# Kernel optimization log

Hardware: AMD Instinct MI355X
Metric: run time of the kernel (lower is better)

## Reference

```python
import jax, jax.numpy as jnp
import numpy as np

NUM_GROUPS = 32
EPS = 1e-5


def setup_inputs() -> dict:
    key = jax.random.key(0)
    ks = jax.random.split(key, 3)
    B, C, H, W = 4, 128, 64, 64
    x = jax.random.normal(ks[0], (B, C, H, W), dtype=jnp.float32)
    norm_w = jnp.ones((C,), jnp.float32)
    norm_b = jnp.zeros((C,), jnp.float32)
    qkv_w = jax.random.normal(ks[1], (3 * C, C), dtype=jnp.float32) * (C ** -0.5)
    qkv_b = jnp.zeros((3 * C,), jnp.float32)
    proj_w = jax.random.normal(ks[2], (C, C), dtype=jnp.float32) * (C ** -0.5)
    proj_b = jnp.zeros((C,), jnp.float32)
    return {"x": x, "norm_w": norm_w, "norm_b": norm_b,
            "qkv_w": qkv_w, "qkv_b": qkv_b,
            "proj_w": proj_w, "proj_b": proj_b}


def group_norm(x, w, b):
    B, C, H, W = x.shape
    xg = x.reshape(B, NUM_GROUPS, -1)  # [B, G, (C/G)*H*W]
    mean = jnp.mean(xg, axis=-1, keepdims=True)
    var = jnp.var(xg, axis=-1, keepdims=True)
    h = ((xg - mean) * jax.lax.rsqrt(var + EPS)).reshape(B, C, H, W)
    return h * w[None, :, None, None] + b[None, :, None, None]


def reference(x, norm_w, norm_b, qkv_w, qkv_b, proj_w, proj_b):
    B, C, H, W = x.shape
    N = H * W
    scale = C ** -0.5
    h = group_norm(x, norm_w, norm_b)
    # 1x1 conv == per-pixel matmul over channels
    qkv = jnp.einsum('bchw,dc->bdhw', h, qkv_w) + qkv_b[None, :, None, None]
    q, k, v = jnp.split(qkv.reshape(B, 3 * C, N), 3, axis=1)  # each [B, C, N]
    attn = jax.nn.softmax(jnp.einsum('bcn,bcm->bnm', q, k) * scale, axis=-1)  # [B,N,N]
    out = jnp.einsum('bnm,bcm->bcn', attn, v).reshape(B, C, H, W)
    out = jnp.einsum('bchw,dc->bdhw', out, proj_w) + proj_b[None, :, None, None]
    return x + out
```

## Files before the change

### kernel.cpp

```cpp
#include <hip/hip_runtime.h>
#include <hip/hip_bf16.h>

typedef __attribute__((ext_vector_type(8))) short short8_t;
typedef __attribute__((ext_vector_type(4))) float f32x4_t;
typedef __attribute__((ext_vector_type(16))) float f32x16_t;
typedef __attribute__((ext_vector_type(2))) unsigned int uint2v_t;
typedef __attribute__((ext_vector_type(4))) unsigned int uint4v_t;

#define MFMA16(a, b, c) __builtin_amdgcn_mfma_f32_16x16x32_bf16((a), (b), (c), 0, 0, 0)
#define MFMA32(a, b, c) __builtin_amdgcn_mfma_f32_32x32x16_bf16((a), (b), (c), 0, 0, 0)

__device__ __forceinline__ unsigned short f2bf(float f) {
  unsigned int u = __float_as_uint(f);
  unsigned int r = (u + 0x7fffu + ((u >> 16) & 1u)) >> 16;
  return (unsigned short)r;
}
__device__ __forceinline__ float bf2f(unsigned short u) {
  return __uint_as_float(((unsigned int)u) << 16);
}

__device__ __forceinline__ unsigned int cvt_pk_bf16(float lo, float hi) {
  unsigned int r;
  asm("v_cvt_pk_bf16_f32 %0, %1, %2" : "=v"(r) : "v"(lo), "v"(hi));
  return r;
}

__device__ __forceinline__ float ex2(float x) {
  float r;
  asm("v_exp_f32 %0, %1" : "=v"(r) : "v"(x));
  return r;
}

__device__ __forceinline__ void gload_lds16(const void* g, void* l) {
  __builtin_amdgcn_global_load_lds(
      (const __attribute__((address_space(1))) unsigned int*)g,
      (__attribute__((address_space(3))) unsigned int*)l, 16, 0, 0);
}

__device__ __forceinline__ void stage_gload_256(const char* __restrict__ g,
                                                char* lds, int nchunks,
                                                int wg, int nw, int lane) {
  for (int c = wg; c < nchunks; c += nw) {
    int row = c * 4 + (lane >> 4);
    int srco = row * 256 + ((((lane & 15) << 4)) ^ ((row & 7) << 4));
    gload_lds16(g + srco, lds + c * 1024);
  }
}

#define NB 4
#define NC 128
#define NN 4096
#define NG 32
#define NS 6
#define ATT_SCALE 0.08838834764831843f
#define QSCALE (0.08838834764831843f * 1.4426950408889634f)
#define FIXED_MAX2 14.426950408889634f

__global__ __launch_bounds__(256) void gn_stats_convw(const float* __restrict__ x,
                                                      const float* __restrict__ qkv_w,
                                                      const float* __restrict__ proj_w,
                                                      float* __restrict__ mean,
                                                      float* __restrict__ rstd,
                                                      unsigned short* __restrict__ wq,
                                                      unsigned short* __restrict__ wp) {
  if (blockIdx.x >= 128) {
    int i = (blockIdx.x - 128) * 256 + threadIdx.x;
    if (i < 384 * 128) wq[i] = f2bf(qkv_w[i]);
    if (i < 128 * 128) wp[i] = f2bf(proj_w[i]);
    return;
  }
  int bg = blockIdx.x;
  const float4* p = (const float4*)(x + (size_t)bg * 16384);
  float s = 0.f, ss = 0.f;
  for (int i = threadIdx.x; i < 4096; i += 256) {
    float4 v = p[i];
    s += v.x + v.y + v.z + v.w;
    ss += v.x * v.x + v.y * v.y + v.z * v.z + v.w * v.w;
  }
#pragma unroll
  for (int off = 32; off >= 1; off >>= 1) {
    s += __shfl_down(s, off);
    ss += __shfl_down(ss, off);
  }
  __shared__ float sb[4], ssb[4];
  int w = threadIdx.x >> 6;
  if ((threadIdx.x & 63) == 0) { sb[w] = s; ssb[w] = ss; }
  __syncthreads();
  if (threadIdx.x == 0) {
    float ts = sb[0] + sb[1] + sb[2] + sb[3];
    float tss = ssb[0] + ssb[1] + ssb[2] + ssb[3];
    float m = ts * (1.f / 16384.f);
    float var = tss * (1.f / 16384.f) - m * m;
    mean[bg] = m;
    rstd[bg] = rsqrtf(var + 1e-5f);
  }
}

__global__ __launch_bounds__(256) void qkv_gemm(const float* __restrict__ x,
                                                const float* __restrict__ mean,
                                                const float* __restrict__ rstd,
                                                const float* __restrict__ gw,
                                                const float* __restrict__ gb,
                                                const unsigned short* __restrict__ wq,
                                                const float* __restrict__ bias,
                                                unsigned short* __restrict__ q_t,
                                                unsigned short* __restrict__ k_t,
                                                unsigned short* __restrict__ v) {
  __shared__ __align__(16) char As[384 * 256];
  __shared__ __align__(16) char Bs[64 * 256];
  __shared__ __align__(16) unsigned short T[128 * 72];
  int nt = blockIdx.x, b = blockIdx.y;
  int tid = threadIdx.x, l = tid & 63, wgv = tid >> 6;
  int n0 = nt * 64;

  stage_gload_256((const char*)wq, As, 96, wgv, 4, l);

  {
    int c = tid >> 1, half = tid & 1;
    int g = c >> 2;
    float m = mean[b * NG + g], rs = rstd[b * NG + g];
    float sc = gw[c] * rs, off = gb[c] - m * sc;
    const float4* xr = (const float4*)(x + (size_t)b * NC * NN + (size_t)c * NN + n0 + half * 32);
    unsigned short* tr = T + c * 72 + half * 32;
#pragma unroll
    for (int j = 0; j < 8; ++j) {
      float4 vv = xr[j];
      unsigned int p0 = (unsigned int)f2bf(vv.x * sc + off) |
                        ((unsigned int)f2bf(vv.y * sc + off) << 16);
      unsigned int p1 = (unsigned int)f2bf(vv.z * sc + off) |
                        ((unsigned int)f2bf(vv.w * sc + off) << 16);
      *(unsigned int*)(tr + j * 4) = p0;
      *(unsigned int*)(tr + j * 4 + 2) = p1;
    }
  }
  __syncthreads();

  for (int u = tid; u < 1024; u += 256) {
    int n = u >> 4, slot = u & 15;
    int c0 = slot * 8;
    uint4 packed;
    packed.x = (unsigned int)T[(c0 + 0) * 72 + n] | ((unsigned int)T[(c0 + 1) * 72 + n] << 16);
    packed.y = (unsigned int)T[(c0 + 2) * 72 + n] | ((unsigned int)T[(c0 + 3) * 72 + n] << 16);
    packed.z = (unsigned int)T[(c0 + 4) * 72 + n] | ((unsigned int)T[(c0 + 5) * 72 + n] << 16);
    packed.w = (unsigned int)T[(c0 + 6) * 72 + n] | ((unsigned int)T[(c0 + 7) * 72 + n] << 16);
    *(uint4*)(Bs + n * 256 + ((slot << 4) ^ ((n & 7) << 4))) = packed;
  }
  __syncthreads();

  int w = tid >> 6;
  int arow0 = w * 32 + (l & 15);
  int brow0 = (l & 15);
  int kbyte0 = (l >> 4) * 16;
  int rbase = (l >> 4) * 4;
  int cl = l & 15;

#pragma unroll
  for (int dt = 0; dt < 3; ++dt) {
    const char* Ad = As + dt * 32768;
    f32x4_t acc[2][4] = {};
#pragma unroll
    for (int kk = 0; kk < 4; ++kk) {
      int kb = kk * 64 + kbyte0;
      short8_t aF[2], bF[4];
#pragma unroll
      for (int mi = 0; mi < 2; ++mi) {
        int r = arow0 + mi * 16;
        aF[mi] = *(const short8_t*)(Ad + r * 256 + (kb ^ ((r & 7) << 4)));
      }
#pragma unroll
      for (int ni = 0; ni < 4; ++ni) {
        int r = brow0 + ni * 16;
        bF[ni] = *(const short8_t*)(Bs + r * 256 + (kb ^ ((r & 7) << 4)));
      }
#pragma unroll
      for (int mi = 0; mi < 2; ++mi)
#pragma unroll
        for (int ni = 0; ni < 4; ++ni)
          acc[mi][ni] = MFMA16(aF[mi], bF[ni], acc[mi][ni]);
    }

#pragma unroll
    for (int mi = 0; mi < 2; ++mi) {
#pragma unroll
      for (int ni = 0; ni < 4; ++ni) {
        int n = n0 + ni * 16 + cl;
#pragma unroll
        for (int r = 0; r < 4; ++r) {
          int d = dt * 128 + w * 32 + mi * 16 + rbase + r;
          float val = acc[mi][ni][r] + bias[d];
          if (dt == 0)
            q_t[((size_t)b * NN + n) * NC + d] = f2bf(val * QSCALE);
          else if (dt == 1)
            k_t[((size_t)b * NN + n) * NC + (d - 128)] = f2bf(val);
          else
            v[((size_t)b * NC + (d - 256)) * NN + n] = f2bf(val);
        }
      }
    }
  }
}

__global__ __launch_bounds__(256) void proj_gemm(const unsigned short* __restrict__ wp,
                                                 const unsigned short* __restrict__ O_p,
                                                 const float* __restrict__ lp,
                                                 const float* __restrict__ bias,
                                                 const float* __restrict__ xres,
                                                 float* __restrict__ out) {
  __shared__ __align__(16) char As[128 * 256];
  __shared__ __align__(16) char Bs[32 * 256];
  __shared__ float invl[32];
  int nt = blockIdx.x, b = blockIdx.z;
  int tid = threadIdx.x, l = tid & 63, wgv = tid >> 6;
  int n0 = nt * 32;

  stage_gload_256((const char*)wp, As, 32, wgv, 4, l);

  if (tid < 32) {
    float ls = 0.f;
#pragma unroll
    for (int s2 = 0; s2 < NS; ++s2)
      ls += lp[(size_t)(b * NS + s2) * NN + n0 + tid];
    invl[tid] = 1.f / ls;
  }
  for (int i = tid; i < 32 * 16; i += 256) {
    int row = i >> 4, sl = i & 15;
    float f[8] = {};
#pragma unroll
    for (int s2 = 0; s2 < NS; ++s2) {
      const unsigned short* p =
          O_p + ((size_t)(b * NS + s2) * NN + n0 + row) * 128 + sl * 8;
      ushort4 u0 = *(const ushort4*)p;
      ushort4 u1 = *(const ushort4*)(p + 4);
      f[0] += bf2f(u0.x); f[1] += bf2f(u0.y); f[2] += bf2f(u0.z); f[3] += bf2f(u0.w);
      f[4] += bf2f(u1.x); f[5] += bf2f(u1.y); f[6] += bf2f(u1.z); f[7] += bf2f(u1.w);
    }
    uint4 packed;
    packed.x = (unsigned int)f2bf(f[0]) | ((unsigned int)f2bf(f[1]) << 16);
    packed.y = (unsigned int)f2bf(f[2]) | ((unsigned int)f2bf(f[3]) << 16);
    packed.z = (unsigned int)f2bf(f[4]) | ((unsigned int)f2bf(f[5]) << 16);
    packed.w = (unsigned int)f2bf(f[6]) | ((unsigned int)f2bf(f[7]) << 16);
    *(uint4*)(Bs + row * 256 + ((sl << 4) ^ ((row & 7) << 4))) = packed;
  }
  __syncthreads();

  int w = tid >> 6;
  f32x4_t acc[2][2] = {};
  int arow0 = w * 32 + (l & 15);
  int brow0 = (l & 15);
  int kbyte0 = (l >> 4) * 16;
#pragma unroll
  for (int kk = 0; kk < 4; ++kk) {
    int kb = kk * 64 + kbyte0;
    short8_t aF[2], bF[2];
#pragma unroll
    for (int mi = 0; mi < 2; ++mi) {
      int r = arow0 + mi * 16;
      aF[mi] = *(const short8_t*)(As + r * 256 + (kb ^ ((r & 7) << 4)));
    }
#pragma unroll
    for (int ni = 0; ni < 2; ++ni) {
      int r = brow0 + ni * 16;
      bF[ni] = *(const short8_t*)(Bs + r * 256 + (kb ^ ((r & 7) << 4)));
    }
#pragma unroll
    for (int mi = 0; mi < 2; ++mi)
#pragma unroll
      for (int ni = 0; ni < 2; ++ni)
        acc[mi][ni] = MFMA16(aF[mi], bF[ni], acc[mi][ni]);
  }

  int rbase = (l >> 4) * 4;
  int cl = l & 15;
  float invl2[2];
#pragma unroll
  for (int ni = 0; ni < 2; ++ni) invl2[ni] = invl[ni * 16 + cl];
#pragma unroll
  for (int mi = 0; mi < 2; ++mi) {
#pragma unroll
    for (int ni = 0; ni < 2; ++ni) {
      int n = n0 + ni * 16 + cl;
#pragma unroll
      for (int r = 0; r < 4; ++r) {
        int d = w * 32 + mi * 16 + rbase + r;
        float val = acc[mi][ni][r] * invl2[ni] + bias[d];
        size_t idx = ((size_t)b * NC + d) * NN + n;
        out[idx] = xres[idx] + val;
      }
    }
  }
}

__device__ __forceinline__ void issue_kv32(const char* __restrict__ gKt,
                                           const char* __restrict__ gVt,
                                           char* Kbuf, char* Vbuf, int wg, int lane) {
#pragma unroll
  for (int i = 0; i < 2; ++i) {
    int ci = wg * 2 + i;
    int row = ci * 4 + (lane >> 4);
    int col = (lane & 15) << 4;
    gload_lds16(gKt + row * 256 + (col ^ ((row & 7) << 4)), Kbuf + ci * 1024);
  }
#pragma unroll
  for (int i = 0; i < 2; ++i) {
    int ci = wg * 2 + i;
    int rowl = lane >> 3;
    int sl = (lane & 7) ^ rowl;
    int c = (ci * 8 + rowl) * 2 + (sl >> 2);
    int k16 = sl & 3;
    gload_lds16(gVt + (size_t)c * (NN * 2) + k16 * 16, Vbuf + ci * 1024);
  }
}

__global__ __launch_bounds__(256, 3) void attn(const unsigned short* __restrict__ q_t,
                                               const unsigned short* __restrict__ k_t,
                                               const unsigned short* __restrict__ v,
                                               unsigned short* __restrict__ O_p,
                                               float* __restrict__ l_p) {
  __shared__ __align__(16) char lds[32768];
  int qt = blockIdx.x, s = blockIdx.y, b = blockIdx.z;
  int tid = threadIdx.x, l = tid & 63, wg = tid >> 6;
  int ql = l & 31, qh = l >> 5;

  int t0 = 21 * s + min(s, 2);
  int cnt = 21 + (s < 2 ? 1 : 0);

  const char* gK = (const char*)(k_t + (size_t)b * NN * NC);
  const char* gV = (const char*)(v + (size_t)b * NC * NN);

  const unsigned short* gQ = q_t + ((size_t)b * NN + qt * 128 + wg * 32) * NC;
  short8_t bQ[8];
#pragma unroll
  for (int kk = 0; kk < 8; ++kk)
    bQ[kk] = *(const short8_t*)(gQ + (size_t)ql * NC + kk * 16 + qh * 8);

  issue_kv32(gK + (size_t)t0 * 8192, gV + (size_t)t0 * 64, lds, lds + 16384, wg, l);
  __syncthreads();

  f32x16_t oacc[4] = {};
  float lsum0 = 0.f, lsum1 = 0.f;

  for (int ti = 0; ti < cnt; ++ti) {
    int co = (ti & 1) << 13;
    int no = co ^ 8192;
    if (ti + 1 < cnt)
      issue_kv32(gK + (size_t)(t0 + ti + 1) * 8192, gV + (size_t)(t0 + ti + 1) * 64,
                 lds + no, lds + 16384 + no, wg, l);
    const char* Ks = lds + co;
    const char* Vs = lds + 16384 + co;

    f32x16_t sacc = {};
    __builtin_amdgcn_s_setprio(1);
#pragma unroll
    for (int kk = 0; kk < 8; ++kk) {
      short8_t aK = *(const short8_t*)(Ks + ql * 256 + ((kk * 32 + qh * 16) ^ ((ql & 7) << 4)));
      sacc = MFMA32(aK, bQ[kk], sacc);
    }
    __builtin_amdgcn_s_setprio(0);

    float p[16];
#pragma unroll
    for (int r = 0; r < 16; ++r) {
      p[r] = ex2(sacc[r] - FIXED_MAX2);
      if (r & 8) lsum1 += p[r]; else lsum0 += p[r];
    }

    unsigned int A0 = cvt_pk_bf16(p[0], p[1]), A1 = cvt_pk_bf16(p[2], p[3]);
    unsigned int B0 = cvt_pk_bf16(p[4], p[5]), B1 = cvt_pk_bf16(p[6], p[7]);
    unsigned int C0 = cvt_pk_bf16(p[8], p[9]), C1 = cvt_pk_bf16(p[10], p[11]);
    unsigned int D0 = cvt_pk_bf16(p[12], p[13]), D1 = cvt_pk_bf16(p[14], p[15]);
    uint2v_t r0 = __builtin_amdgcn_permlane32_swap(A0, B0, false, false);
    uint2v_t r1 = __builtin_amdgcn_permlane32_swap(A1, B1, false, false);
    uint2v_t r2 = __builtin_amdgcn_permlane32_swap(C0, D0, false, false);
    uint2v_t r3 = __builtin_amdgcn_permlane32_swap(C1, D1, false, false);
    uint4v_t pa0 = {r0.x, r1.x, r0.y, r1.y};
    uint4v_t pa1 = {r2.x, r3.x, r2.y, r3.y};
    short8_t PA0 = __builtin_bit_cast(short8_t, pa0);
    short8_t PA1 = __builtin_bit_cast(short8_t, pa1);

    __builtin_amdgcn_s_setprio(1);
#pragma unroll
    for (int cb = 0; cb < 4; ++cb) {
#pragma unroll
      for (int ks = 0; ks < 2; ++ks) {
        int c = cb * 32 + ql;
        int row = c >> 1;
        int sl = ((c & 1) << 2) | (ks << 1) | qh;
        int pp = sl ^ (row & 7);
        short8_t aV = *(const short8_t*)(Vs + row * 128 + pp * 16);
        oacc[cb] = MFMA32(ks ? PA1 : PA0, aV, oacc[cb]);
      }
    }
    __builtin_amdgcn_s_setprio(0);

    __syncthreads();
  }

  float lanesum = lsum0 + lsum1;
  lanesum += __shfl_xor(lanesum, 32);

  unsigned short* Ob = O_p + ((size_t)(b * NS + s) * NN + qt * 128 + wg * 32) * 128;
#pragma unroll
  for (int r = 0; r < 16; ++r) {
    int q = (r & 3) + 8 * (r >> 2) + 4 * qh;
#pragma unroll
    for (int cb = 0; cb < 4; ++cb)
      Ob[(size_t)q * 128 + cb * 32 + ql] = f2bf(oacc[cb][r]);
  }
  if (l < 32)
    l_p[(size_t)(b * NS + s) * NN + qt * 128 + wg * 32 + ql] = lanesum;
}

extern "C" void kernel_launch(void* const* d_in, const int* in_sizes, int n_in,
                              void* d_out, int out_size, void* d_ws, size_t ws_size,
                              hipStream_t stream) {
  const float* x = (const float*)d_in[0];
  const float* norm_w = (const float*)d_in[1];
  const float* norm_b = (const float*)d_in[2];
  const float* qkv_w = (const float*)d_in[3];
  const float* qkv_b = (const float*)d_in[4];
  const float* proj_w = (const float*)d_in[5];
  const float* proj_b = (const float*)d_in[6];
  float* out = (float*)d_out;

  char* ws = (char*)d_ws;
  float* mean = (float*)ws;
  float* rstd = (float*)(ws + 512);
  unsigned short* wq = (unsigned short*)(ws + 4096);
  unsigned short* wp = (unsigned short*)(ws + 4096 + 98304);
  const size_t TEN = (size_t)NB * NN * NC;
  unsigned short* q_t = (unsigned short*)(ws + (1 << 18));
  unsigned short* k_t = q_t + TEN;
  unsigned short* v = k_t + TEN;
  unsigned short* O_p = (unsigned short*)(ws + (1 << 18) + 3 * TEN * 2);
  float* l_p = (float*)((char*)O_p + (size_t)NS * NB * NN * NC * 2);

  gn_stats_convw<<<320, 256, 0, stream>>>(x, qkv_w, proj_w, mean, rstd, wq, wp);
  qkv_gemm<<<dim3(NN / 64, NB), 256, 0, stream>>>(x, mean, rstd, norm_w, norm_b,
                                                  wq, qkv_b, q_t, k_t, v);
  attn<<<dim3(NN / 128, NS, NB), 256, 0, stream>>>(q_t, k_t, v, O_p, l_p);
  proj_gemm<<<dim3(NN / 32, 1, NB), 256, 0, stream>>>(wp, O_p, l_p, proj_b, x, out);
}
```

Before: 69.55 us.

## Shrink QKV and proj GEMM tiles to 16 columns, read weights directly from global

Both the QKV and projection GEMM kernels now process 16 pixels per block instead of 64/32, launching 4x/2x more blocks. The LDS staging of the full bf16 weight matrix is dropped; each wave reads its A fragments straight from global memory, which should be served mostly from L2. The goal is to cut the large LDS footprint (about 112 KB in qkv_gemm) and the per-block weight staging cost, so that more blocks fit per CU and occupancy rises. In exchange, weight traffic from global/L2 grows, each B fragment is reused across fewer MFMAs, and output stores come in smaller, less coalesced chunks.

```diff
diff --git a/kernel.cpp b/kernel.cpp
--- a/kernel.cpp
+++ b/kernel.cpp
@@ -35,16 +35,6 @@
   __builtin_amdgcn_global_load_lds(
       (const __attribute__((address_space(1))) unsigned int*)g,
       (__attribute__((address_space(3))) unsigned int*)l, 16, 0, 0);
-}
-
-__device__ __forceinline__ void stage_gload_256(const char* __restrict__ g,
-                                                char* lds, int nchunks,
-                                                int wg, int nw, int lane) {
-  for (int c = wg; c < nchunks; c += nw) {
-    int row = c * 4 + (lane >> 4);
-    int srco = row * 256 + ((((lane & 15) << 4)) ^ ((row & 7) << 4));
-    gload_lds16(g + srco, lds + c * 1024);
-  }
 }
 
 #define NB 4
@@ -106,24 +96,21 @@
                                                 unsigned short* __restrict__ q_t,
                                                 unsigned short* __restrict__ k_t,
                                                 unsigned short* __restrict__ v) {
-  __shared__ __align__(16) char As[384 * 256];
-  __shared__ __align__(16) char Bs[64 * 256];
-  __shared__ __align__(16) unsigned short T[128 * 72];
+  __shared__ __align__(16) char Bs[16 * 256];
+  __shared__ __align__(16) unsigned short T[128 * 20];
   int nt = blockIdx.x, b = blockIdx.y;
-  int tid = threadIdx.x, l = tid & 63, wgv = tid >> 6;
-  int n0 = nt * 64;
-
-  stage_gload_256((const char*)wq, As, 96, wgv, 4, l);
+  int tid = threadIdx.x, l = tid & 63;
+  int n0 = nt * 16;
 
   {
     int c = tid >> 1, half = tid & 1;
     int g = c >> 2;
     float m = mean[b * NG + g], rs = rstd[b * NG + g];
     float sc = gw[c] * rs, off = gb[c] - m * sc;
-    const float4* xr = (const float4*)(x + (size_t)b * NC * NN + (size_t)c * NN + n0 + half * 32);
-    unsigned short* tr = T + c * 72 + half * 32;
-#pragma unroll
-    for (int j = 0; j < 8; ++j) {
+    const float4* xr = (const float4*)(x + (size_t)b * NC * NN + (size_t)c * NN + n0 + half * 8);
+    unsigned short* tr = T + c * 20 + half * 8;
+#pragma unroll
+    for (int j = 0; j < 2; ++j) {
       float4 vv = xr[j];
       unsigned int p0 = (unsigned int)f2bf(vv.x * sc + off) |
                         ((unsigned int)f2bf(vv.y * sc + off) << 16);
@@ -135,66 +122,55 @@
   }
   __syncthreads();
 
-  for (int u = tid; u < 1024; u += 256) {
-    int n = u >> 4, slot = u & 15;
+  {
+    int n = tid >> 4, slot = tid & 15;
     int c0 = slot * 8;
     uint4 packed;
-    packed.x = (unsigned int)T[(c0 + 0) * 72 + n] | ((unsigned int)T[(c0 + 1) * 72 + n] << 16);
-    packed.y = (unsigned int)T[(c0 + 2) * 72 + n] | ((unsigned int)T[(c0 + 3) * 72 + n] << 16);
-    packed.z = (unsigned int)T[(c0 + 4) * 72 + n] | ((unsigned int)T[(c0 + 5) * 72 + n] << 16);
-    packed.w = (unsigned int)T[(c0 + 6) * 72 + n] | ((unsigned int)T[(c0 + 7) * 72 + n] << 16);
+    packed.x = (unsigned int)T[(c0 + 0) * 20 + n] | ((unsigned int)T[(c0 + 1) * 20 + n] << 16);
+    packed.y = (unsigned int)T[(c0 + 2) * 20 + n] | ((unsigned int)T[(c0 + 3) * 20 + n] << 16);
+    packed.z = (unsigned int)T[(c0 + 4) * 20 + n] | ((unsigned int)T[(c0 + 5) * 20 + n] << 16);
+    packed.w = (unsigned int)T[(c0 + 6) * 20 + n] | ((unsigned int)T[(c0 + 7) * 20 + n] << 16);
     *(uint4*)(Bs + n * 256 + ((slot << 4) ^ ((n & 7) << 4))) = packed;
   }
   __syncthreads();
 
   int w = tid >> 6;
-  int arow0 = w * 32 + (l & 15);
-  int brow0 = (l & 15);
-  int kbyte0 = (l >> 4) * 16;
-  int rbase = (l >> 4) * 4;
+  int arow_l = l & 15;
+  int kq = l >> 4;
+  int rbase = kq * 4;
   int cl = l & 15;
 
 #pragma unroll
   for (int dt = 0; dt < 3; ++dt) {
-    const char* Ad = As + dt * 32768;
-    f32x4_t acc[2][4] = {};
+    f32x4_t acc[2] = {};
 #pragma unroll
     for (int kk = 0; kk < 4; ++kk) {
-      int kb = kk * 64 + kbyte0;
-      short8_t aF[2], bF[4];
+      short8_t aF[2], bF;
 #pragma unroll
       for (int mi = 0; mi < 2; ++mi) {
-        int r = arow0 + mi * 16;
-        aF[mi] = *(const short8_t*)(Ad + r * 256 + (kb ^ ((r & 7) << 4)));
+        int r = dt * 128 + w * 32 + mi * 16 + arow_l;
+        aF[mi] = *(const short8_t*)(wq + (size_t)r * NC + kk * 32 + kq * 8);
       }
-#pragma unroll
-      for (int ni = 0; ni < 4; ++ni) {
-        int r = brow0 + ni * 16;
-        bF[ni] = *(const short8_t*)(Bs + r * 256 + (kb ^ ((r & 7) << 4)));
-      }
+      int rr = arow_l;
+      bF = *(const short8_t*)(Bs + rr * 256 + ((kk * 64 + kq * 16) ^ ((rr & 7) << 4)));
 #pragma unroll
       for (int mi = 0; mi < 2; ++mi)
-#pragma unroll
-        for (int ni = 0; ni < 4; ++ni)
-          acc[mi][ni] = MFMA16(aF[mi], bF[ni], acc[mi][ni]);
+        acc[mi] = MFMA16(aF[mi], bF, acc[mi]);
     }
 
 #pragma unroll
     for (int mi = 0; mi < 2; ++mi) {
-#pragma unroll
-      for (int ni = 0; ni < 4; ++ni) {
-        int n = n0 + ni * 16 + cl;
-#pragma unroll
-        for (int r = 0; r < 4; ++r) {
-          int d = dt * 128 + w * 32 + mi * 16 + rbase + r;
-          float val = acc[mi][ni][r] + bias[d];
-          if (dt == 0)
-            q_t[((size_t)b * NN + n) * NC + d] = f2bf(val * QSCALE);
-          else if (dt == 1)
-            k_t[((size_t)b * NN + n) * NC + (d - 128)] = f2bf(val);
-          else
-            v[((size_t)b * NC + (d - 256)) * NN + n] = f2bf(val);
-        }
+      int n = n0 + cl;
+#pragma unroll
+      for (int r = 0; r < 4; ++r) {
+        int d = dt * 128 + w * 32 + mi * 16 + rbase + r;
+        float val = acc[mi][r] + bias[d];
+        if (dt == 0)
+          q_t[((size_t)b * NN + n) * NC + d] = f2bf(val * QSCALE);
+        else if (dt == 1)
+          k_t[((size_t)b * NN + n) * NC + (d - 128)] = f2bf(val);
+        else
+          v[((size_t)b * NC + (d - 256)) * NN + n] = f2bf(val);
       }
     }
   }
@@ -206,24 +182,21 @@
                                                  const float* __restrict__ bias,
                                                  const float* __restrict__ xres,
                                                  float* __restrict__ out) {
-  __shared__ __align__(16) char As[128 * 256];
-  __shared__ __align__(16) char Bs[32 * 256];
-  __shared__ float invl[32];
-  int nt = blockIdx.x, b = blockIdx.z;
-  int tid = threadIdx.x, l = tid & 63, wgv = tid >> 6;
-  int n0 = nt * 32;
-
-  stage_gload_256((const char*)wp, As, 32, wgv, 4, l);
-
-  if (tid < 32) {
+  __shared__ __align__(16) char Bs[16 * 256];
+  __shared__ float invl[16];
+  int nt = blockIdx.x, b = blockIdx.y;
+  int tid = threadIdx.x, l = tid & 63;
+  int n0 = nt * 16;
+
+  if (tid < 16) {
     float ls = 0.f;
 #pragma unroll
     for (int s2 = 0; s2 < NS; ++s2)
       ls += lp[(size_t)(b * NS + s2) * NN + n0 + tid];
     invl[tid] = 1.f / ls;
   }
-  for (int i = tid; i < 32 * 16; i += 256) {
-    int row = i >> 4, sl = i & 15;
+  {
+    int row = tid >> 4, sl = tid & 15;
     float f[8] = {};
 #pragma unroll
     for (int s2 = 0; s2 < NS; ++s2) {
@@ -244,48 +217,36 @@
   __syncthreads();
 
   int w = tid >> 6;
-  f32x4_t acc[2][2] = {};
-  int arow0 = w * 32 + (l & 15);
-  int brow0 = (l & 15);
-  int kbyte0 = (l >> 4) * 16;
+  int arow_l = l & 15;
+  int kq = l >> 4;
+  f32x4_t acc[2] = {};
 #pragma unroll
   for (int kk = 0; kk < 4; ++kk) {
-    int kb = kk * 64 + kbyte0;
-    short8_t aF[2], bF[2];
+    short8_t aF[2], bF;
 #pragma unroll
     for (int mi = 0; mi < 2; ++mi) {
-      int r = arow0 + mi * 16;
-      aF[mi] = *(const short8_t*)(As + r * 256 + (kb ^ ((r & 7) << 4)));
-    }
-#pragma unroll
-    for (int ni = 0; ni < 2; ++ni) {
-      int r = brow0 + ni * 16;
-      bF[ni] = *(const short8_t*)(Bs + r * 256 + (kb ^ ((r & 7) << 4)));
-    }
+      int r = w * 32 + mi * 16 + arow_l;
+      aF[mi] = *(const short8_t*)(wp + (size_t)r * NC + kk * 32 + kq * 8);
+    }
+    int rr = arow_l;
+    bF = *(const short8_t*)(Bs + rr * 256 + ((kk * 64 + kq * 16) ^ ((rr & 7) << 4)));
 #pragma unroll
     for (int mi = 0; mi < 2; ++mi)
-#pragma unroll
-      for (int ni = 0; ni < 2; ++ni)
-        acc[mi][ni] = MFMA16(aF[mi], bF[ni], acc[mi][ni]);
-  }
-
-  int rbase = (l >> 4) * 4;
+      acc[mi] = MFMA16(aF[mi], bF, acc[mi]);
+  }
+
+  int rbase = kq * 4;
   int cl = l & 15;
-  float invl2[2];
-#pragma unroll
-  for (int ni = 0; ni < 2; ++ni) invl2[ni] = invl[ni * 16 + cl];
+  float invl_c = invl[cl];
 #pragma unroll
   for (int mi = 0; mi < 2; ++mi) {
-#pragma unroll
-    for (int ni = 0; ni < 2; ++ni) {
-      int n = n0 + ni * 16 + cl;
-#pragma unroll
-      for (int r = 0; r < 4; ++r) {
-        int d = w * 32 + mi * 16 + rbase + r;
-        float val = acc[mi][ni][r] * invl2[ni] + bias[d];
-        size_t idx = ((size_t)b * NC + d) * NN + n;
-        out[idx] = xres[idx] + val;
-      }
+    int n = n0 + cl;
+#pragma unroll
+    for (int r = 0; r < 4; ++r) {
+      int d = w * 32 + mi * 16 + rbase + r;
+      float val = acc[mi][r] * invl_c + bias[d];
+      size_t idx = ((size_t)b * NC + d) * NN + n;
+      out[idx] = xres[idx] + val;
     }
   }
 }
@@ -435,8 +396,8 @@
   float* l_p = (float*)((char*)O_p + (size_t)NS * NB * NN * NC * 2);
 
   gn_stats_convw<<<320, 256, 0, stream>>>(x, qkv_w, proj_w, mean, rstd, wq, wp);
-  qkv_gemm<<<dim3(NN / 64, NB), 256, 0, stream>>>(x, mean, rstd, norm_w, norm_b,
+  qkv_gemm<<<dim3(NN / 16, NB), 256, 0, stream>>>(x, mean, rstd, norm_w, norm_b,
                                                   wq, qkv_b, q_t, k_t, v);
   attn<<<dim3(NN / 128, NS, NB), 256, 0, stream>>>(q_t, k_t, v, O_p, l_p);
-  proj_gemm<<<dim3(NN / 32, 1, NB), 256, 0, stream>>>(wp, O_p, l_p, proj_b, x, out);
-}
+  proj_gemm<<<dim3(NN / 16, NB), 256, 0, stream>>>(wp, O_p, l_p, proj_b, x, out);
+}
```

New measurement: 77.15 us. 1.11x slower.
